# Kernel optimization log

Hardware: AMD Instinct MI355X
Metric: run time of the kernel (lower is better)

The kernel has to match this reference:

```python
import jax, jax.numpy as jnp
import numpy as np
from jax import lax

T = 256          # sentence length
WD, TD = 300, 100  # word/tag embedding dims
H = WD + TD      # LSTM hidden (=input) size, per module __init__
VOCAB, NTAGS = 50000, 50
MLP_H = 400


def setup_inputs() -> dict:
    key = jax.random.key(0)
    ks = jax.random.split(key, 20)
    s = 0.05  # small init scale for numerical stability
    return {
        "words": jax.random.randint(ks[0], (T,), 0, VOCAB),
        "tags": jax.random.randint(ks[1], (T,), 0, NTAGS),
        "word_emb": jax.random.normal(ks[2], (VOCAB, WD), jnp.float32),
        "tag_emb": jax.random.normal(ks[3], (NTAGS, TD), jnp.float32),
        "Wih0": jax.random.normal(ks[4], (2, 4 * H, H), jnp.float32) * s,
        "Whh0": jax.random.normal(ks[5], (2, 4 * H, H), jnp.float32) * s,
        "bih0": jax.random.normal(ks[6], (2, 4 * H), jnp.float32) * s,
        "bhh0": jax.random.normal(ks[7], (2, 4 * H), jnp.float32) * s,
        "Wih1": jax.random.normal(ks[8], (2, 4 * H, 2 * H), jnp.float32) * s,
        "Whh1": jax.random.normal(ks[9], (2, 4 * H, H), jnp.float32) * s,
        "bih1": jax.random.normal(ks[10], (2, 4 * H), jnp.float32) * s,
        "bhh1": jax.random.normal(ks[11], (2, 4 * H), jnp.float32) * s,
        "W1": jax.random.normal(ks[12], (MLP_H, 4 * H), jnp.float32) * s,
        "b1": jax.random.normal(ks[13], (MLP_H,), jnp.float32) * s,
        "W2": jax.random.normal(ks[14], (1, MLP_H), jnp.float32) * s,
        "b2": jax.random.normal(ks[15], (1,), jnp.float32) * s,
        "h0": jax.random.normal(ks[16], (2, 2, H), jnp.float32),  # [layer, dir, H]
        "c0": jax.random.normal(ks[17], (2, 2, H), jnp.float32),
    }


def _lstm_dir(xs, Wih, Whh, bih, bhh, h0, c0, reverse):
    # xs: [T, D]; torch LSTM gate order i, f, g, o
    def step(carry, xt):
        h, c = carry
        g = xt @ Wih.T + bih + h @ Whh.T + bhh  # [4H]
        i, f, gg, o = jnp.split(g, 4)
        c = jax.nn.sigmoid(f) * c + jax.nn.sigmoid(i) * jnp.tanh(gg)
        h = jax.nn.sigmoid(o) * jnp.tanh(c)
        return (h, c), h
    _, hs = lax.scan(step, (h0, c0), xs, reverse=reverse)
    return hs  # [T, H]


def _forward(words, tags, word_emb, tag_emb, Wih0, Whh0, bih0, bhh0,
             Wih1, Whh1, bih1, bhh1, W1, b1, W2, b2, h0, c0):
    x = jnp.concatenate([word_emb[words], tag_emb[tags]], axis=1)  # [T, H]
    # layer 0, both directions
    hf0 = _lstm_dir(x, Wih0[0], Whh0[0], bih0[0], bhh0[0], h0[0, 0], c0[0, 0], False)
    hb0 = _lstm_dir(x, Wih0[1], Whh0[1], bih0[1], bhh0[1], h0[0, 1], c0[0, 1], True)
    x1 = jnp.concatenate([hf0, hb0], axis=1)  # [T, 2H]
    # layer 1
    hf1 = _lstm_dir(x1, Wih1[0], Whh1[0], bih1[0], bhh1[0], h0[1, 0], c0[1, 0], False)
    hb1 = _lstm_dir(x1, Wih1[1], Whh1[1], bih1[1], bhh1[1], h0[1, 1], c0[1, 1], True)
    hvec = jnp.concatenate([hf1, hb1], axis=1)  # [T, 2H]
    # batched pairwise MLP: score(i,j) = W2 @ tanh(W1 @ [h_i; h_j] + b1) + b2
    # Split W1 so the concat is never materialized over all T^2 pairs.
    W1a, W1b = W1[:, :2 * H], W1[:, 2 * H:]
    pi = hvec @ W1a.T  # [T, MLP_H] contribution of head word i
    pj = hvec @ W1b.T  # [T, MLP_H] contribution of dependent word j
    act = jnp.tanh(pi[:, None, :] + pj[None, :, :] + b1)  # [T, T, MLP_H]
    scores = act @ W2[0] + b2[0]  # [T, T]
    # diagonal stays 0 (permutations exclude i == j; scoreTensor was zeroed)
    return scores * (1.0 - jnp.eye(T, dtype=scores.dtype))


def reference(words, tags, word_emb, tag_emb, Wih0, Whh0, bih0, bhh0,
              Wih1, Whh1, bih1, bhh1, W1, b1, W2, b2, h0, c0):
    return _forward(words, tags, word_emb, tag_emb, Wih0, Whh0, bih0, bhh0,
                    Wih1, Whh1, bih1, bhh1, W1, b1, W2, b2, h0, c0)
```

## Files before the change

### kernel.cpp

```cpp
#include <hip/hip_runtime.h>
#include <hip/hip_bf16.h>

#define T 256
#define H 400
#define G4 1600
#define WD 300
#define TD 100
#define MLP_H 400
#define NBLK_D 25
#define HB 16
#define GR 64
#define WSTR 202
#define NPAIR 200

typedef _Float16 f16;
typedef _Float16 half2t __attribute__((ext_vector_type(2)));
typedef unsigned long long u64;
typedef unsigned int u32;

__device__ __forceinline__ float fexp(float x) {
    return __builtin_amdgcn_exp2f(x * 1.4426950408889634f);
}
__device__ __forceinline__ float sigf(float x) {
    return __builtin_amdgcn_rcpf(1.0f + fexp(-x));
}
__device__ __forceinline__ float tanhf_fast(float x) {
    return 1.0f - 2.0f * __builtin_amdgcn_rcpf(1.0f + fexp(2.0f * x));
}
__device__ __forceinline__ unsigned short f16bits(f16 x) {
    union { f16 h; unsigned short u; } v; v.h = x; return v.u;
}
__device__ __forceinline__ u32 packh2(float a, float b) {
    half2t hv; hv.x = (_Float16)a; hv.y = (_Float16)b;
    return __builtin_bit_cast(u32, hv);
}

#if __has_builtin(__builtin_amdgcn_fdot2)
__device__ __forceinline__ float dot2u(u32 a, u32 b, float c) {
    return __builtin_amdgcn_fdot2(__builtin_bit_cast(half2t, a),
                                  __builtin_bit_cast(half2t, b), c, false);
}
#else
__device__ __forceinline__ float dot2u(u32 a, u32 b, float c) {
    half2t x = __builtin_bit_cast(half2t, a), y = __builtin_bit_cast(half2t, b);
    return fmaf((float)x.y, (float)y.y, fmaf((float)x.x, (float)y.x, c));
}
#endif

__device__ __forceinline__ u64 sysload(const u64* p) {
    return __hip_atomic_load(p, __ATOMIC_RELAXED, __HIP_MEMORY_SCOPE_SYSTEM);
}
__device__ __forceinline__ void sysstore(u64* p, u64 v) {
    __hip_atomic_store(p, v, __ATOMIC_RELAXED, __HIP_MEMORY_SCOPE_SYSTEM);
}

__global__ __launch_bounds__(256) void gemm_l0(
    const int* __restrict__ words, const int* __restrict__ tags,
    const float* __restrict__ wemb, const float* __restrict__ temb,
    const float* __restrict__ Wt,
    const float* __restrict__ bias1,
    const float* __restrict__ bias2,
    float* __restrict__ out,
    const float* __restrict__ h0, u64* sA, u64* sB) {
    const int tid = threadIdx.x;
    const int z = blockIdx.z;
    const int t0 = blockIdx.x * 64, r0 = blockIdx.y * 64;

    if (r0 >= G4) {
        if (blockIdx.x != 0 || z != 0) return;
        const int TOT = 2 * 2 * NPAIR;
        for (int i = tid; i < TOT; i += 256) { sA[i] = 0xFFFFULL; sB[i] = 0xFFFFULL; }
        __syncthreads();
        for (int p = tid; p < 2 * NPAIR; p += 256) {
            int d = p / NPAIR, pr = p - d * NPAIR;
            size_t off = (size_t)(d * 2 + 0) * NPAIR + pr;
            f16 a0 = (f16)h0[d * H + 2 * pr], b0 = (f16)h0[d * H + 2 * pr + 1];
            sA[off] = 0ULL | ((u64)f16bits(a0) << 16) | ((u64)f16bits(b0) << 32);
            f16 a1 = (f16)h0[2 * H + d * H + 2 * pr], b1 = (f16)h0[2 * H + d * H + 2 * pr + 1];
            sB[off] = 0ULL | ((u64)f16bits(a1) << 16) | ((u64)f16bits(b1) << 32);
        }
        return;
    }

    __shared__ float Xs[2][64][17];
    __shared__ float Ws[2][64][17];
    __shared__ int wsh[64], tsh[64];
    const float* Wtz = Wt + (size_t)z * G4 * H;
    const float* b1 = bias1 + (size_t)z * G4;
    const float* b2 = bias2 + (size_t)z * G4;
    float* outz = out + (size_t)z * T * G4;
    const int lr = tid >> 2, kq = (tid & 3) * 4;
    const int ti = tid >> 4, rj = tid & 15;
    if (tid < 64) { wsh[tid] = words[t0 + tid]; tsh[tid] = tags[t0 + tid]; }
    __syncthreads();
    {
        float4 xv = (kq < WD)
            ? *(const float4*)(wemb + (size_t)wsh[lr] * WD + kq)
            : *(const float4*)(temb + (size_t)tsh[lr] * TD + (kq - WD));
        Xs[0][lr][kq + 0] = xv.x; Xs[0][lr][kq + 1] = xv.y;
        Xs[0][lr][kq + 2] = xv.z; Xs[0][lr][kq + 3] = xv.w;
        float4 wv = *(const float4*)(Wtz + (size_t)(r0 + lr) * H + kq);
        Ws[0][lr][kq + 0] = wv.x; Ws[0][lr][kq + 1] = wv.y;
        Ws[0][lr][kq + 2] = wv.z; Ws[0][lr][kq + 3] = wv.w;
    }
    __syncthreads();
    float acc[4][4] = {};
    const int niter = H / 16;
    for (int it = 0; it < niter; ++it) {
        const int buf = it & 1;
        const bool more = (it + 1 < niter);
        float4 xn, wn;
        if (more) {
            int k = ((it + 1) << 4) + kq;
            xn = (k < WD)
                ? *(const float4*)(wemb + (size_t)wsh[lr] * WD + k)
                : *(const float4*)(temb + (size_t)tsh[lr] * TD + (k - WD));
            wn = *(const float4*)(Wtz + (size_t)(r0 + lr) * H + k);
        }
#pragma unroll
        for (int kk = 0; kk < 16; kk++) {
            float xr[4], wr[4];
#pragma unroll
            for (int m = 0; m < 4; m++) xr[m] = Xs[buf][ti * 4 + m][kk];
#pragma unroll
            for (int n = 0; n < 4; n++) wr[n] = Ws[buf][rj * 4 + n][kk];
#pragma unroll
            for (int m = 0; m < 4; m++)
#pragma unroll
                for (int n = 0; n < 4; n++)
                    acc[m][n] = fmaf(xr[m], wr[n], acc[m][n]);
        }
        if (more) {
            Xs[buf ^ 1][lr][kq + 0] = xn.x; Xs[buf ^ 1][lr][kq + 1] = xn.y;
            Xs[buf ^ 1][lr][kq + 2] = xn.z; Xs[buf ^ 1][lr][kq + 3] = xn.w;
            Ws[buf ^ 1][lr][kq + 0] = wn.x; Ws[buf ^ 1][lr][kq + 1] = wn.y;
            Ws[buf ^ 1][lr][kq + 2] = wn.z; Ws[buf ^ 1][lr][kq + 3] = wn.w;
        }
        __syncthreads();
    }
    int rq = r0 + rj * 4;
    {
        float b[4];
#pragma unroll
        for (int n = 0; n < 4; n++) { int r = rq + n; b[n] = b1[r] + b2[r]; }
#pragma unroll
        for (int m = 0; m < 4; m++) {
            int t = t0 + ti * 4 + m;
            float4 o;
            o.x = acc[m][0] + b[0]; o.y = acc[m][1] + b[1];
            o.z = acc[m][2] + b[2]; o.w = acc[m][3] + b[3];
            *(float4*)(outz + (size_t)t * G4 + rq) = o;
        }
    }
}

__global__ __launch_bounds__(256) void gemm_tnz(
    const float* __restrict__ X, int ldx,
    const float* __restrict__ Wt, long wz, int ldw, int wofs0, int wstep,
    const float* __restrict__ bias1, int b1zs, int b1mask,
    const float* __restrict__ bias2, int b2zs, int b2mask,
    float* __restrict__ out, int ldo, long ozs, int Rt, int K) {
    __shared__ float Xs[2][64][17];
    __shared__ float Ws[2][64][17];
    const int tid = threadIdx.x;
    const int z = blockIdx.z;
    const float* Wtz = Wt + (size_t)z * wz;
    const int wofs = wofs0 + z * wstep;
    const float* b1 = (bias1 && ((b1mask >> z) & 1)) ? bias1 + (size_t)z * b1zs : nullptr;
    const float* b2 = (bias2 && ((b2mask >> z) & 1)) ? bias2 + (size_t)z * b2zs : nullptr;
    float* outz = out + (size_t)z * ozs;
    const int t0 = blockIdx.x * 64, r0 = blockIdx.y * 64;
    const int lr = tid >> 2, kq = (tid & 3) * 4;
    const int ti = tid >> 4, rj = tid & 15;
    {
        float4 xv = *(const float4*)(X + (size_t)(t0 + lr) * ldx + kq);
        Xs[0][lr][kq + 0] = xv.x; Xs[0][lr][kq + 1] = xv.y;
        Xs[0][lr][kq + 2] = xv.z; Xs[0][lr][kq + 3] = xv.w;
        int r = r0 + lr;
        float4 wv = make_float4(0.f, 0.f, 0.f, 0.f);
        if (r < Rt) wv = *(const float4*)(Wtz + (size_t)r * ldw + wofs + kq);
        Ws[0][lr][kq + 0] = wv.x; Ws[0][lr][kq + 1] = wv.y;
        Ws[0][lr][kq + 2] = wv.z; Ws[0][lr][kq + 3] = wv.w;
    }
    __syncthreads();
    float acc[4][4] = {};
    const int niter = K >> 4;
    for (int it = 0; it < niter; ++it) {
        const int buf = it & 1;
        const bool more = (it + 1 < niter);
        float4 xn, wn;
        if (more) {
            int k0 = (it + 1) << 4;
            xn = *(const float4*)(X + (size_t)(t0 + lr) * ldx + k0 + kq);
            int r = r0 + lr;
            wn = make_float4(0.f, 0.f, 0.f, 0.f);
            if (r < Rt) wn = *(const float4*)(Wtz + (size_t)r * ldw + wofs + k0 + kq);
        }
#pragma unroll
        for (int kk = 0; kk < 16; kk++) {
            float xr[4], wr[4];
#pragma unroll
            for (int m = 0; m < 4; m++) xr[m] = Xs[buf][ti * 4 + m][kk];
#pragma unroll
            for (int n = 0; n < 4; n++) wr[n] = Ws[buf][rj * 4 + n][kk];
#pragma unroll
            for (int m = 0; m < 4; m++)
#pragma unroll
                for (int n = 0; n < 4; n++)
                    acc[m][n] = fmaf(xr[m], wr[n], acc[m][n]);
        }
        if (more) {
            Xs[buf ^ 1][lr][kq + 0] = xn.x; Xs[buf ^ 1][lr][kq + 1] = xn.y;
            Xs[buf ^ 1][lr][kq + 2] = xn.z; Xs[buf ^ 1][lr][kq + 3] = xn.w;
            Ws[buf ^ 1][lr][kq + 0] = wn.x; Ws[buf ^ 1][lr][kq + 1] = wn.y;
            Ws[buf ^ 1][lr][kq + 2] = wn.z; Ws[buf ^ 1][lr][kq + 3] = wn.w;
        }
        __syncthreads();
    }
    int rq = r0 + rj * 4;
    if (rq < Rt) {
        float b[4];
#pragma unroll
        for (int n = 0; n < 4; n++) {
            int r = rq + n;
            b[n] = (b1 ? b1[r] : 0.f) + (b2 ? b2[r] : 0.f);
        }
#pragma unroll
        for (int m = 0; m < 4; m++) {
            int t = t0 + ti * 4 + m;
            float4 o;
            o.x = acc[m][0] + b[0]; o.y = acc[m][1] + b[1];
            o.z = acc[m][2] + b[2]; o.w = acc[m][3] + b[3];
            *(float4*)(outz + (size_t)t * ldo + rq) = o;
        }
    }
}

__global__ __launch_bounds__(512, 1) void lstm_layer8(
    const float* __restrict__ G,
    const float* __restrict__ Whh,
    const float* __restrict__ c0l,
    float* __restrict__ xout,
    u64* __restrict__ slots) {
    const int role = blockIdx.x;
    const int dir = role / NBLK_D, blk = role - dir * NBLK_D;
    const int tid = threadIdx.x;
    const float* Wd = Whh + (size_t)dir * G4 * H;
    const float* Gd = G + (size_t)dir * T * G4;
    u64* sd = slots + (size_t)dir * 2 * NPAIR;

    __shared__ u32 wlds[GR * WSTR];
    __shared__ __align__(16) u32 hsh[NPAIR];
    __shared__ float gsum[GR];
    __shared__ float gsh[2][GR];

    for (int idx = tid; idx < GR * 100; idx += 512) {
        int row = idx / 100, c4 = idx - row * 100;
        int g = row >> 4, r = row & 15;
        const float4* src = (const float4*)(Wd + (size_t)(g * H + blk * HB + r) * H);
        float4 f = src[c4];
        *(uint2*)&wlds[row * WSTR + c4 * 2] =
            make_uint2(packh2(f.x, f.y), packh2(f.z, f.w));
    }
    if (tid >= 448) {
        int i = tid - 448, gg = i >> 4, rr = i & 15;
        int tt0 = dir ? (T - 1) : 0;
        gsh[0][i] = Gd[(size_t)tt0 * G4 + gg * H + blk * HB + rr];
    } else if (tid < 8) {
        u64 v = sysload(sd + blk * 8 + tid);
        hsh[blk * 8 + tid] = (u32)(v >> 16);
    }
    float c = (tid < 64) ? c0l[dir * H + blk * HB + (tid & 15)] : 0.f;
    __syncthreads();

#pragma clang loop unroll(disable)
    for (int s = 0; s < T; ++s) {
        if (tid >= 256 && tid < 448) {
            int f = tid - 256;
            int widx = f + (f >= blk * 8 ? 8 : 0);
            u64* src = sd + (size_t)(s & 1) * NPAIR + widx;
            u64 v = sysload(src);
            int spins = 0;
            while ((unsigned)(v & 0xFFFFULL) != (unsigned)s) {
                if (++spins > 16384) {
                    v = __hip_atomic_fetch_add(src, 0ULL, __ATOMIC_RELAXED,
                                               __HIP_MEMORY_SCOPE_AGENT);
                } else {
                    v = sysload(src);
                }
            }
            hsh[widx] = (u32)(v >> 16);
        } else if (tid >= 448) {
            int sn = (s + 1 < T) ? (s + 1) : s;
            int tt = dir ? (T - 1 - sn) : sn;
            int i = tid - 448, gg = i >> 4, rr = i & 15;
            gsh[(s + 1) & 1][i] = Gd[(size_t)tt * G4 + gg * H + blk * HB + rr];
        }
        __syncthreads();

        if (tid < 256) {
            const int row = tid >> 2, sl = tid & 3;
            const u32* wp = &wlds[row * WSTR + sl * 50];
            const u32* hp = &hsh[sl * 50];
            float a0 = 0.f, a1 = 0.f, a2 = 0.f, a3 = 0.f;
#pragma unroll
            for (int i = 0; i < 12; ++i) {
                uint2 wv0 = *(const uint2*)&wp[4 * i];
                uint2 hv0 = *(const uint2*)&hp[4 * i];
                uint2 wv1 = *(const uint2*)&wp[4 * i + 2];
                uint2 hv1 = *(const uint2*)&hp[4 * i + 2];
                a0 = dot2u(wv0.x, hv0.x, a0);
                a1 = dot2u(wv0.y, hv0.y, a1);
                a2 = dot2u(wv1.x, hv1.x, a2);
                a3 = dot2u(wv1.y, hv1.y, a3);
            }
            {
                uint2 wv = *(const uint2*)&wp[48];
                uint2 hv = *(const uint2*)&hp[48];
                a0 = dot2u(wv.x, hv.x, a0);
                a1 = dot2u(wv.y, hv.y, a1);
            }
            float a = (a0 + a1) + (a2 + a3);
            a += __shfl_xor(a, 1);
            a += __shfl_xor(a, 2);
            if (sl == 0) gsum[row] = a;
        }
        __syncthreads();

        if (tid < 64) {
            const int r = tid & 15;
            const float* gc = gsh[s & 1];
            float iv = gsum[r]      + gc[r];
            float fv = gsum[16 + r] + gc[16 + r];
            float gv = gsum[32 + r] + gc[32 + r];
            float ov = gsum[48 + r] + gc[48 + r];
            float cn = sigf(fv) * c + sigf(iv) * tanhf_fast(gv);
            c = cn;
            float hn = sigf(ov) * tanhf_fast(cn);
            u32 hb = (u32)f16bits((f16)hn);
            u32 lo = __shfl(hb, (2 * tid) & 63);
            u32 hi = __shfl(hb, (2 * tid + 1) & 63);
            if (tid < 8) {
                u32 pk = (lo & 0xFFFFu) | (hi << 16);
                hsh[blk * 8 + tid] = pk;
                sysstore(sd + (size_t)((s + 1) & 1) * NPAIR + blk * 8 + tid,
                         (u64)(unsigned)(s + 1) | ((u64)pk << 16));
            }
            const int tt = dir ? (T - 1 - s) : s;
            if (tid < 16)
                xout[(size_t)tt * (2 * H) + dir * H + blk * HB + tid] = hn;
        }
    }
}

__global__ __launch_bounds__(256) void scores_k(
    const float* __restrict__ pi, const float* __restrict__ pj,
    const float* __restrict__ w2, const float* __restrict__ b2p,
    float* __restrict__ out) {
    __shared__ float Ps[16][401];
    __shared__ float Qs[16][401];
    __shared__ float w2s[400];
    const int tid = threadIdx.x;
    const int i0 = blockIdx.y * 16, j0 = blockIdx.x * 16;
    for (int r = 0; r < 16; r++) {
        for (int k = tid; k < MLP_H; k += 256) {
            Ps[r][k] = pi[(size_t)(i0 + r) * MLP_H + k];
            Qs[r][k] = pj[(size_t)(j0 + r) * MLP_H + k];
        }
    }
    for (int k = tid; k < MLP_H; k += 256) w2s[k] = w2[k];
    __syncthreads();
    const int ti = tid >> 4, tj = tid & 15;
    float acc = 0.f;
#pragma unroll 4
    for (int k = 0; k < MLP_H; k++) {
        float x = Ps[ti][k] + Qs[tj][k];
        acc = fmaf(w2s[k], tanhf_fast(x), acc);
    }
    const int i = i0 + ti, j = j0 + tj;
    out[(size_t)i * T + j] = (i == j) ? 0.f : (acc + b2p[0]);
}

extern "C" void kernel_launch(void* const* d_in, const int* in_sizes, int n_in,
                              void* d_out, int out_size, void* d_ws, size_t ws_size,
                              hipStream_t stream) {
    const int*   words = (const int*)d_in[0];
    const int*   tags  = (const int*)d_in[1];
    const float* wemb  = (const float*)d_in[2];
    const float* temb  = (const float*)d_in[3];
    const float* Wih0  = (const float*)d_in[4];
    const float* Whh0  = (const float*)d_in[5];
    const float* bih0  = (const float*)d_in[6];
    const float* bhh0  = (const float*)d_in[7];
    const float* Wih1  = (const float*)d_in[8];
    const float* Whh1  = (const float*)d_in[9];
    const float* bih1  = (const float*)d_in[10];
    const float* bhh1  = (const float*)d_in[11];
    const float* W1    = (const float*)d_in[12];
    const float* b1    = (const float*)d_in[13];
    const float* W2    = (const float*)d_in[14];
    const float* b2    = (const float*)d_in[15];
    const float* h0    = (const float*)d_in[16];
    const float* c0    = (const float*)d_in[17];
    float* out = (float*)d_out;

    float* W = (float*)d_ws;
    float* x1   = W + 102400;
    float* hvec = W + 307200;
    float* Gb   = W + 512000;
    float* pi   = W + 1331200;
    float* pj   = W + 1433600;
    u64* slotsA = (u64*)W;
    u64* slotsB = (u64*)(W + 2048);

    gemm_l0<<<dim3(4, 26, 2), 256, 0, stream>>>(
        words, tags, wemb, temb, Wih0, bih0, bhh0, Gb, h0, slotsA, slotsB);

    lstm_layer8<<<2 * NBLK_D, 512, 0, stream>>>(Gb, Whh0, c0, x1, slotsA);

    gemm_tnz<<<dim3(4, 25, 2), 256, 0, stream>>>(
        x1, 2 * H, Wih1, (long)G4 * 2 * H, 2 * H, 0, 0,
        bih1, G4, 3, bhh1, G4, 3,
        Gb, G4, (long)T * G4, G4, 2 * H);

    lstm_layer8<<<2 * NBLK_D, 512, 0, stream>>>(Gb, Whh1, c0 + 2 * H, hvec, slotsB);

    gemm_tnz<<<dim3(4, 7, 2), 256, 0, stream>>>(
        hvec, 2 * H, W1, 0L, G4, 0, 2 * H,
        b1, 0, 1, nullptr, 0, 0,
        pi, MLP_H, 102400L, MLP_H, 2 * H);

    scores_k<<<dim3(16, 16), 256, 0, stream>>>(pi, pj, W2, b2, out);
}
```

Baseline: 1.261 ms.

## Interleave forward and backward LSTM directions within each block to hide sync latency

```diff
diff --git a/kernel.cpp b/kernel.cpp
--- a/kernel.cpp
+++ b/kernel.cpp
@@ -7,7 +7,7 @@
 #define WD 300
 #define TD 100
 #define MLP_H 400
-#define NBLK_D 25
+#define NBLK 25
 #define HB 16
 #define GR 64
 #define WSTR 202
@@ -236,119 +236,154 @@
     }
 }
 
-__global__ __launch_bounds__(512, 1) void lstm_layer8(
+__global__ __launch_bounds__(512, 1) void lstm_layer_dual(
     const float* __restrict__ G,
     const float* __restrict__ Whh,
     const float* __restrict__ c0l,
     float* __restrict__ xout,
     u64* __restrict__ slots) {
-    const int role = blockIdx.x;
-    const int dir = role / NBLK_D, blk = role - dir * NBLK_D;
+    const int blk = blockIdx.x;
     const int tid = threadIdx.x;
-    const float* Wd = Whh + (size_t)dir * G4 * H;
-    const float* Gd = G + (size_t)dir * T * G4;
-    u64* sd = slots + (size_t)dir * 2 * NPAIR;
-
-    __shared__ u32 wlds[GR * WSTR];
-    __shared__ __align__(16) u32 hsh[NPAIR];
+    u64* sdF = slots;
+    u64* sdB = slots + 2 * NPAIR;
+
+    __shared__ u32 wlds[2][GR * WSTR];
+    __shared__ __align__(16) u32 hshF[NPAIR];
+    __shared__ __align__(16) u32 hshB[NPAIR];
     __shared__ float gsum[GR];
-    __shared__ float gsh[2][GR];
-
-    for (int idx = tid; idx < GR * 100; idx += 512) {
-        int row = idx / 100, c4 = idx - row * 100;
+    __shared__ float gshF[2][GR];
+    __shared__ float gshB[2][GR];
+    __shared__ u32 wflag[4];
+
+    for (int idx = tid; idx < 2 * GR * 100; idx += 512) {
+        int d = idx / (GR * 100), rem = idx - d * (GR * 100);
+        int row = rem / 100, c4 = rem - row * 100;
         int g = row >> 4, r = row & 15;
-        const float4* src = (const float4*)(Wd + (size_t)(g * H + blk * HB + r) * H);
+        const float4* src = (const float4*)(
+            Whh + (size_t)d * G4 * H + (size_t)(g * H + blk * HB + r) * H);
         float4 f = src[c4];
-        *(uint2*)&wlds[row * WSTR + c4 * 2] =
+        *(uint2*)&wlds[d][row * WSTR + c4 * 2] =
             make_uint2(packh2(f.x, f.y), packh2(f.z, f.w));
     }
+    if (tid < 4) wflag[tid] = 0xFFFFFFFFu;
     if (tid >= 448) {
         int i = tid - 448, gg = i >> 4, rr = i & 15;
-        int tt0 = dir ? (T - 1) : 0;
-        gsh[0][i] = Gd[(size_t)tt0 * G4 + gg * H + blk * HB + rr];
+        gshF[0][i] = G[(size_t)0 * G4 + gg * H + blk * HB + rr];
+        gshB[0][i] = G[((size_t)T + (T - 1)) * G4 + gg * H + blk * HB + rr];
     } else if (tid < 8) {
-        u64 v = sysload(sd + blk * 8 + tid);
-        hsh[blk * 8 + tid] = (u32)(v >> 16);
-    }
-    float c = (tid < 64) ? c0l[dir * H + blk * HB + (tid & 15)] : 0.f;
+        u64 v = sysload(sdF + blk * 8 + tid);
+        hshF[blk * 8 + tid] = (u32)(v >> 16);
+    } else if (tid < 16) {
+        u64 v = sysload(sdB + blk * 8 + (tid - 8));
+        hshB[blk * 8 + (tid - 8)] = (u32)(v >> 16);
+    } else if (tid >= 256 && tid < 448) {
+        int f = tid - 256;
+        int widx = f + (f >= blk * 8 ? 8 : 0);
+        u64* src = sdF + widx;
+        u64 v = sysload(src);
+        int spins = 0;
+        while ((unsigned)(v & 0xFFFFULL) != 0u) {
+            if (++spins > 16384) {
+                v = __hip_atomic_fetch_add(src, 0ULL, __ATOMIC_RELAXED,
+                                           __HIP_MEMORY_SCOPE_AGENT);
+            } else {
+                v = sysload(src);
+            }
+        }
+        hshF[widx] = (u32)(v >> 16);
+    }
+    float cf = (tid < 64) ? c0l[blk * HB + (tid & 15)] : 0.f;
+    float cb = (tid < 64) ? c0l[H + blk * HB + (tid & 15)] : 0.f;
     __syncthreads();
 
 #pragma clang loop unroll(disable)
     for (int s = 0; s < T; ++s) {
-        if (tid >= 256 && tid < 448) {
-            int f = tid - 256;
-            int widx = f + (f >= blk * 8 ? 8 : 0);
-            u64* src = sd + (size_t)(s & 1) * NPAIR + widx;
-            u64 v = sysload(src);
-            int spins = 0;
-            while ((unsigned)(v & 0xFFFFULL) != (unsigned)s) {
-                if (++spins > 16384) {
-                    v = __hip_atomic_fetch_add(src, 0ULL, __ATOMIC_RELAXED,
-                                               __HIP_MEMORY_SCOPE_AGENT);
-                } else {
-                    v = sysload(src);
+#pragma clang loop unroll(disable)
+        for (int d = 0; d < 2; ++d) {
+            const u32 p = (u32)(2 * s + d);
+            if (tid < 256) {
+                const int row = tid >> 2, sl = tid & 3;
+                const u32* wp = &wlds[d][row * WSTR + sl * 50];
+                const u32* hp = &(d ? hshB : hshF)[sl * 50];
+                float a0 = 0.f, a1 = 0.f, a2 = 0.f, a3 = 0.f;
+#pragma unroll
+                for (int i = 0; i < 12; ++i) {
+                    uint2 wv0 = *(const uint2*)&wp[4 * i];
+                    uint2 hv0 = *(const uint2*)&hp[4 * i];
+                    uint2 wv1 = *(const uint2*)&wp[4 * i + 2];
+                    uint2 hv1 = *(const uint2*)&hp[4 * i + 2];
+                    a0 = dot2u(wv0.x, hv0.x, a0);
+                    a1 = dot2u(wv0.y, hv0.y, a1);
+                    a2 = dot2u(wv1.x, hv1.x, a2);
+                    a3 = dot2u(wv1.y, hv1.y, a3);
                 }
+                {
+                    uint2 wv = *(const uint2*)&wp[48];
+                    uint2 hv = *(const uint2*)&hp[48];
+                    a0 = dot2u(wv.x, hv.x, a0);
+                    a1 = dot2u(wv.y, hv.y, a1);
+                }
+                float a = (a0 + a1) + (a2 + a3);
+                a += __shfl_xor(a, 1);
+                a += __shfl_xor(a, 2);
+                if (sl == 0) gsum[row] = a;
+                asm volatile("s_waitcnt lgkmcnt(0)" ::: "memory");
+                if ((tid & 63) == 0) wflag[tid >> 6] = p;
+                if (tid < 64) {
+                    {
+                        const volatile u32* vf = wflag;
+                        while (!((vf[1] == p) && (vf[2] == p) && (vf[3] == p))) {}
+                    }
+                    asm volatile("" ::: "memory");
+                    const int r = tid & 15;
+                    const float* gc = (d ? gshB : gshF)[s & 1];
+                    float iv = gsum[r]      + gc[r];
+                    float fv = gsum[16 + r] + gc[16 + r];
+                    float gv = gsum[32 + r] + gc[32 + r];
+                    float ov = gsum[48 + r] + gc[48 + r];
+                    float c = d ? cb : cf;
+                    float cn = sigf(fv) * c + sigf(iv) * tanhf_fast(gv);
+                    if (d) cb = cn; else cf = cn;
+                    float hn = sigf(ov) * tanhf_fast(cn);
+                    u32 hb = (u32)f16bits((f16)hn);
+                    u32 lo = __shfl(hb, (2 * tid) & 63);
+                    u32 hi = __shfl(hb, (2 * tid + 1) & 63);
+                    if (tid < 8) {
+                        u32 pk = (lo & 0xFFFFu) | (hi << 16);
+                        (d ? hshB : hshF)[blk * 8 + tid] = pk;
+                        sysstore((d ? sdB : sdF) + (size_t)((s + 1) & 1) * NPAIR + blk * 8 + tid,
+                                 (u64)(unsigned)(s + 1) | ((u64)pk << 16));
+                    }
+                    const int tt = d ? (T - 1 - s) : s;
+                    if (tid < 16)
+                        xout[(size_t)tt * (2 * H) + d * H + blk * HB + tid] = hn;
+                }
+            } else if (tid < 448) {
+                int f = tid - 256;
+                int widx = f + (f >= blk * 8 ? 8 : 0);
+                int tg = (d == 0) ? s : (s + 1);
+                if (tg < T) {
+                    u64* src = (d == 0 ? sdB : sdF) + (size_t)(tg & 1) * NPAIR + widx;
+                    u64 v = sysload(src);
+                    int spins = 0;
+                    while ((unsigned)(v & 0xFFFFULL) != (unsigned)tg) {
+                        if (++spins > 16384) {
+                            v = __hip_atomic_fetch_add(src, 0ULL, __ATOMIC_RELAXED,
+                                                       __HIP_MEMORY_SCOPE_AGENT);
+                        } else {
+                            v = sysload(src);
+                        }
+                    }
+                    (d == 0 ? hshB : hshF)[widx] = (u32)(v >> 16);
+                }
+            } else {
+                int sn = (s + 1 < T) ? (s + 1) : s;
+                int tt = d ? (T - 1 - sn) : sn;
+                int i = tid - 448, gg = i >> 4, rr = i & 15;
+                (d ? gshB : gshF)[(s + 1) & 1][i] =
+                    G[((size_t)d * T + tt) * G4 + gg * H + blk * HB + rr];
             }
-            hsh[widx] = (u32)(v >> 16);
-        } else if (tid >= 448) {
-            int sn = (s + 1 < T) ? (s + 1) : s;
-            int tt = dir ? (T - 1 - sn) : sn;
-            int i = tid - 448, gg = i >> 4, rr = i & 15;
-            gsh[(s + 1) & 1][i] = Gd[(size_t)tt * G4 + gg * H + blk * HB + rr];
-        }
-        __syncthreads();
-
-        if (tid < 256) {
-            const int row = tid >> 2, sl = tid & 3;
-            const u32* wp = &wlds[row * WSTR + sl * 50];
-            const u32* hp = &hsh[sl * 50];
-            float a0 = 0.f, a1 = 0.f, a2 = 0.f, a3 = 0.f;
-#pragma unroll
-            for (int i = 0; i < 12; ++i) {
-                uint2 wv0 = *(const uint2*)&wp[4 * i];
-                uint2 hv0 = *(const uint2*)&hp[4 * i];
-                uint2 wv1 = *(const uint2*)&wp[4 * i + 2];
-                uint2 hv1 = *(const uint2*)&hp[4 * i + 2];
-                a0 = dot2u(wv0.x, hv0.x, a0);
-                a1 = dot2u(wv0.y, hv0.y, a1);
-                a2 = dot2u(wv1.x, hv1.x, a2);
-                a3 = dot2u(wv1.y, hv1.y, a3);
-            }
-            {
-                uint2 wv = *(const uint2*)&wp[48];
-                uint2 hv = *(const uint2*)&hp[48];
-                a0 = dot2u(wv.x, hv.x, a0);
-                a1 = dot2u(wv.y, hv.y, a1);
-            }
-            float a = (a0 + a1) + (a2 + a3);
-            a += __shfl_xor(a, 1);
-            a += __shfl_xor(a, 2);
-            if (sl == 0) gsum[row] = a;
-        }
-        __syncthreads();
-
-        if (tid < 64) {
-            const int r = tid & 15;
-            const float* gc = gsh[s & 1];
-            float iv = gsum[r]      + gc[r];
-            float fv = gsum[16 + r] + gc[16 + r];
-            float gv = gsum[32 + r] + gc[32 + r];
-            float ov = gsum[48 + r] + gc[48 + r];
-            float cn = sigf(fv) * c + sigf(iv) * tanhf_fast(gv);
-            c = cn;
-            float hn = sigf(ov) * tanhf_fast(cn);
-            u32 hb = (u32)f16bits((f16)hn);
-            u32 lo = __shfl(hb, (2 * tid) & 63);
-            u32 hi = __shfl(hb, (2 * tid + 1) & 63);
-            if (tid < 8) {
-                u32 pk = (lo & 0xFFFFu) | (hi << 16);
-                hsh[blk * 8 + tid] = pk;
-                sysstore(sd + (size_t)((s + 1) & 1) * NPAIR + blk * 8 + tid,
-                         (u64)(unsigned)(s + 1) | ((u64)pk << 16));
-            }
-            const int tt = dir ? (T - 1 - s) : s;
-            if (tid < 16)
-                xout[(size_t)tt * (2 * H) + dir * H + blk * HB + tid] = hn;
+            __syncthreads();
         }
     }
 }
@@ -416,14 +451,14 @@
     gemm_l0<<<dim3(4, 26, 2), 256, 0, stream>>>(
         words, tags, wemb, temb, Wih0, bih0, bhh0, Gb, h0, slotsA, slotsB);
 
-    lstm_layer8<<<2 * NBLK_D, 512, 0, stream>>>(Gb, Whh0, c0, x1, slotsA);
+    lstm_layer_dual<<<NBLK, 512, 0, stream>>>(Gb, Whh0, c0, x1, slotsA);
 
     gemm_tnz<<<dim3(4, 25, 2), 256, 0, stream>>>(
         x1, 2 * H, Wih1, (long)G4 * 2 * H, 2 * H, 0, 0,
         bih1, G4, 3, bhh1, G4, 3,
         Gb, G4, (long)T * G4, G4, 2 * H);
 
-    lstm_layer8<<<2 * NBLK_D, 512, 0, stream>>>(Gb, Whh1, c0 + 2 * H, hvec, slotsB);
+    lstm_layer_dual<<<NBLK, 512, 0, stream>>>(Gb, Whh1, c0 + 2 * H, hvec, slotsB);
 
     gemm_tnz<<<dim3(4, 7, 2), 256, 0, stream>>>(
         hvec, 2 * H, W1, 0L, G4, 0, 2 * H,
```

After: 1.477 ms. 17.2% more time.
